# Optimization experiments

Measured on AMD Instinct MI355X. Metric: run time of the kernel, lower is better.

Reference implementation:

```python
import jax, jax.numpy as jnp
import numpy as np

EMBED = 768
HEADS = 12
HEAD_DIM = EMBED // HEADS

def setup_inputs() -> dict:
    key = jax.random.key(0)
    k1, k2, k3, k4 = jax.random.split(key, 4)
    x = jax.random.normal(k1, (8, 1024, EMBED), dtype=jnp.float32)
    # qkv Linear (no bias per qkv_bias=False); proj Linear with bias
    w_qkv = jax.random.normal(k2, (EMBED, 3 * EMBED), dtype=jnp.float32) * 0.02
    w_proj = jax.random.normal(k3, (EMBED, EMBED), dtype=jnp.float32) * 0.02
    b_proj = jax.random.normal(k4, (EMBED,), dtype=jnp.float32) * 0.02
    return {"x": x, "w_qkv": w_qkv, "w_proj": w_proj, "b_proj": b_proj}

def reference(x, w_qkv, w_proj, b_proj):
    b, n, e = x.shape
    h, d = HEADS, HEAD_DIM
    scale = d ** (-0.5)
    qkv = x @ w_qkv                                    # [b, n, 3*e]
    qkv = qkv.reshape(b, n, 3, h, d)                   # (qkv h d) split order
    q, k, v = (jnp.transpose(qkv[:, :, i], (0, 2, 1, 3)) for i in range(3))  # [b,h,n,d]
    dots = jnp.einsum('bhid,bhjd->bhij', q, k) * scale
    attn = jax.nn.softmax(dots, axis=-1)               # dropout p=0 -> identity
    out = jnp.einsum('bhij,bhjd->bhid', attn, v)       # [b,h,n,d]
    out = jnp.transpose(out, (0, 2, 1, 3)).reshape(b, n, e)
    return out @ w_proj + b_proj
```

## Files before the change

kernel.cpp:

```cpp
#include <hip/hip_runtime.h>

typedef _Float16 f16;
typedef _Float16 half8 __attribute__((ext_vector_type(8)));
typedef _Float16 half4v __attribute__((ext_vector_type(4)));
typedef __fp16 fp16x2 __attribute__((ext_vector_type(2)));
typedef float f32x4 __attribute__((ext_vector_type(4)));
typedef float f32x16 __attribute__((ext_vector_type(16)));
typedef unsigned uint4v __attribute__((ext_vector_type(4)));

#define MFMA16(a,b,c) __builtin_amdgcn_mfma_f32_16x16x32_f16((a),(b),(c),0,0,0)
#define MFMA32(a,b,c) __builtin_amdgcn_mfma_f32_32x32x16_f16((a),(b),(c),0,0,0)

__device__ __forceinline__ void gload_lds16(const f16* g, f16* l) {
    __builtin_amdgcn_global_load_lds(
        (const __attribute__((address_space(1))) unsigned int*)g,
        (__attribute__((address_space(3))) unsigned int*)l, 16, 0, 0);
}

__device__ __forceinline__ void plswap(unsigned &a, unsigned &b) {
    asm volatile("v_permlane32_swap_b32 %0, %1" : "+v"(a), "+v"(b));
}

__device__ __forceinline__ unsigned pk2(float a, float b) {
    return __builtin_bit_cast(unsigned, __builtin_amdgcn_cvt_pkrtz(a, b));
}

__device__ __forceinline__ float fexp2(float x) {
#if __has_builtin(__builtin_amdgcn_exp2f)
    return __builtin_amdgcn_exp2f(x);
#else
    return exp2f(x);
#endif
}

__device__ __forceinline__ float xswap32(float x, int hi) {
    unsigned a = __builtin_bit_cast(unsigned, x), b = a;
    asm volatile("v_permlane32_swap_b32 %0, %1" : "+v"(a), "+v"(b));
    return __builtin_bit_cast(float, hi ? a : b);
}

__global__ void cast_f32_to_f16(const float* __restrict__ in, f16* __restrict__ out, int n4) {
    int i = blockIdx.x * blockDim.x + threadIdx.x;
    if (i < n4) {
        float4 v = ((const float4*)in)[i];
        half4v h;
        h.x = (f16)v.x; h.y = (f16)v.y; h.z = (f16)v.z; h.w = (f16)v.w;
        ((half4v*)out)[i] = h;
    }
}

__global__ void transpose_cast(const float* __restrict__ in, f16* __restrict__ out, int K, int N) {
    __shared__ f16 tile[32][33];
    int n0 = blockIdx.x * 32, k0 = blockIdx.y * 32;
    int tx = threadIdx.x & 31, ty = threadIdx.x >> 5;
    for (int r = ty; r < 32; r += 8)
        tile[r][tx] = (f16)in[(size_t)(k0 + r) * N + (n0 + tx)];
    __syncthreads();
    for (int r = ty; r < 32; r += 8)
        out[(size_t)(n0 + r) * K + (k0 + tx)] = tile[tx][r];
}

__global__ __launch_bounds__(256, 3)
void gemm_qkv(const f16* __restrict__ A, const f16* __restrict__ Bt,
              f16* __restrict__ qbuf, f16* __restrict__ kbuf, f16* __restrict__ vtbuf)
{
    constexpr int K = 768;
    constexpr int NX = 18;
    constexpr int NWG = NX * 64;
    __shared__ __align__(16) char smem[49152];
    f16* As = (f16*)smem;
    f16* Bs = (f16*)(smem + 24576);
    const int tid  = threadIdx.x;
    const int lane = tid & 63, wave = tid >> 6;
    const int wm = wave >> 1, wn = wave & 1;
    const int l15 = lane & 15, l4 = lane >> 4;

    const int bid = blockIdx.x;
    const int swz = (bid & 7) * (NWG / 8) + (bid >> 3);
    const int m0 = (swz / NX) * 128, n0 = (swz % NX) * 128;

    const int srow  = lane >> 2;
    const int sslot = lane & 3;

    f32x4 acc[4][4] = {};

    #define GSTAGE(buf, kt) do {                                                     \
        _Pragma("unroll")                                                            \
        for (int i = 0; i < 2; ++i) {                                                \
            int rbase = i * 64 + wave * 16;                                          \
            int row = rbase + srow;                                                  \
            gload_lds16(A  + (size_t)(m0 + row) * K + (kt) + sslot * 8, &As[(buf) * 4096 + rbase * 32]); \
            gload_lds16(Bt + (size_t)(n0 + row) * K + (kt) + sslot * 8, &Bs[(buf) * 4096 + rbase * 32]); \
        }                                                                            \
    } while (0)

    GSTAGE(0, 0);
    GSTAGE(1, 32);

    int cur = 0;
    for (int t = 0; t < 24; ++t) {
        if (t < 23) asm volatile("s_waitcnt vmcnt(4)" ::: "memory");
        else        asm volatile("s_waitcnt vmcnt(0)" ::: "memory");
        __builtin_amdgcn_s_barrier();
        if (t < 22) {
            int nb = cur + 2; if (nb >= 3) nb -= 3;
            GSTAGE(nb, (t + 2) * 32);
        }
        half8 af[4], bf[4];
        #pragma unroll
        for (int mi = 0; mi < 4; mi++) af[mi] = *(const half8*)&As[cur*4096 + (wm*64 + mi*16 + l15) * 32 + l4*8];
        #pragma unroll
        for (int ni = 0; ni < 4; ni++) bf[ni] = *(const half8*)&Bs[cur*4096 + (wn*64 + ni*16 + l15) * 32 + l4*8];
        #pragma unroll
        for (int mi = 0; mi < 4; mi++)
            #pragma unroll
            for (int ni = 0; ni < 4; ni++)
                acc[mi][ni] = MFMA16(af[mi], bf[ni], acc[mi][ni]);
        if (++cur >= 3) cur = 0;
    }
    #undef GSTAGE

    __syncthreads();
    f16* sC = (f16*)smem;
    const int t3 = n0 / 768;
    const int bb = m0 >> 10;
    const int mo = m0 & 1023;
    const int h0 = (n0 - t3 * 768) >> 6;

    if (t3 < 2) {
        #pragma unroll
        for (int mi = 0; mi < 4; mi++)
            #pragma unroll
            for (int ni = 0; ni < 4; ni++)
                #pragma unroll
                for (int r = 0; r < 4; r++) {
                    int row = wm*64 + mi*16 + l4*4 + r;
                    int col = wn*64 + ni*16 + l15;
                    sC[row * 136 + col] = (f16)acc[mi][ni][r];
                }
        __syncthreads();
        f16* outb = (t3 == 0) ? qbuf : kbuf;
        #pragma unroll
        for (int hc = 0; hc < 2; hc++) {
            f16* base = outb + ((size_t)(bb * 12 + h0 + hc) * 1024 + mo) * 64;
            #pragma unroll
            for (int i = 0; i < 4; i++) {
                int row = wave * 32 + i * 8 + (lane >> 3);
                int cc  = (lane & 7) * 8;
                half8 v = *(const half8*)&sC[row * 136 + hc * 64 + cc];
                *(half8*)(base + row * 64 + cc) = v;
            }
        }
    } else {
        #pragma unroll
        for (int mi = 0; mi < 4; mi++)
            #pragma unroll
            for (int ni = 0; ni < 4; ni++) {
                int row0 = wm*64 + mi*16 + l4*4;
                int col  = wn*64 + ni*16 + l15;
                half4v pk;
                #pragma unroll
                for (int r = 0; r < 4; r++) pk[r] = (f16)acc[mi][ni][r];
                *(half4v*)&sC[col * 136 + row0] = pk;
            }
        __syncthreads();
        #pragma unroll
        for (int i = 0; i < 8; i++) {
            int col = wave * 32 + i * 4 + (lane >> 4);
            int rc  = (lane & 15) * 8;
            half8 v = *(const half8*)&sC[col * 136 + rc];
            int head = h0 + (col >> 6), dd = col & 63;
            *(half8*)(vtbuf + ((size_t)(bb * 12 + head) * 64 + dd) * 1024 + mo + rc) = v;
        }
    }
}

__global__ __launch_bounds__(256, 4)
void gemm_proj(const f16* __restrict__ A, const f16* __restrict__ Bt,
               float* __restrict__ out, const float* __restrict__ bias)
{
    constexpr int K = 768;
    constexpr int NX = 12;
    constexpr int NWG = 64 * NX;
    __shared__ __align__(16) char smem[36864];
    f16* As = (f16*)smem;
    f16* Bs = (f16*)(smem + 24576);
    const int tid  = threadIdx.x;
    const int lane = tid & 63, wave = tid >> 6;
    const int wm = wave >> 1, wn = wave & 1;
    const int l15 = lane & 15, l4 = lane >> 4;

    const int bid = blockIdx.x;
    const int swz = (bid & 7) * (NWG / 8) + (bid >> 3);
    const int m0 = (swz / NX) * 128, n0 = (swz % NX) * 64;

    const int srow  = lane >> 2;
    const int sslot = lane & 3;

    f32x4 acc[4][2] = {};

    #define GSTAGE(buf, kt) do {                                                     \
        _Pragma("unroll")                                                            \
        for (int i = 0; i < 2; ++i) {                                                \
            int rbase = i * 64 + wave * 16;                                          \
            gload_lds16(A + (size_t)(m0 + rbase + srow) * K + (kt) + sslot * 8,      \
                        &As[(buf) * 4096 + rbase * 32]);                             \
        }                                                                            \
        gload_lds16(Bt + (size_t)(n0 + wave * 16 + srow) * K + (kt) + sslot * 8,     \
                    &Bs[(buf) * 2048 + wave * 16 * 32]);                             \
    } while (0)

    GSTAGE(0, 0);
    GSTAGE(1, 32);

    int cur = 0;
    for (int t = 0; t < 24; ++t) {
        if (t < 23) asm volatile("s_waitcnt vmcnt(3)" ::: "memory");
        else        asm volatile("s_waitcnt vmcnt(0)" ::: "memory");
        __builtin_amdgcn_s_barrier();
        if (t < 22) {
            int nb = cur + 2; if (nb >= 3) nb -= 3;
            GSTAGE(nb, (t + 2) * 32);
        }
        half8 af[4], bf[2];
        #pragma unroll
        for (int mi = 0; mi < 4; mi++) af[mi] = *(const half8*)&As[cur*4096 + (wm*64 + mi*16 + l15) * 32 + l4*8];
        #pragma unroll
        for (int ni = 0; ni < 2; ni++) bf[ni] = *(const half8*)&Bs[cur*2048 + (wn*32 + ni*16 + l15) * 32 + l4*8];
        #pragma unroll
        for (int mi = 0; mi < 4; mi++)
            #pragma unroll
            for (int ni = 0; ni < 2; ni++)
                acc[mi][ni] = MFMA16(af[mi], bf[ni], acc[mi][ni]);
        if (++cur >= 3) cur = 0;
    }
    #undef GSTAGE

    #pragma unroll
    for (int mi = 0; mi < 4; mi++)
        #pragma unroll
        for (int ni = 0; ni < 2; ni++)
            #pragma unroll
            for (int r = 0; r < 4; r++) {
                int gm = m0 + wm*64 + mi*16 + l4*4 + r;
                int gn = n0 + wn*32 + ni*16 + l15;
                out[(size_t)gm * 768 + gn] = acc[mi][ni][r] + bias[gn];
            }
}

__global__ __launch_bounds__(256, 3)
void attn_kernel(const f16* __restrict__ qbuf, const f16* __restrict__ kbuf,
                 const f16* __restrict__ vtbuf, f16* __restrict__ obuf)
{
    __shared__ __align__(16) f16 Ks[3][4096];
    __shared__ __align__(16) f16 Vs[3][4096];
    const int tid = threadIdx.x;
    const int lane = tid & 63, wave = tid >> 6;
    const int bh = blockIdx.x;
    const int b = bh / 12, h = bh % 12;
    const int q0 = blockIdx.y * 128 + wave * 32;
    const int l31 = lane & 31, hi = lane >> 5;
    const int sw0 = (l31 & 7) << 4;

    const f16* Q  = qbuf  + (size_t)bh * 65536;
    const f16* Kp = kbuf  + (size_t)bh * 65536;
    const f16* Vt = vtbuf + (size_t)bh * 65536;

    const f16 slh = (f16)(0.125f * 1.44269504089f);
    half8 aq[4];
    #pragma unroll
    for (int c = 0; c < 4; c++) {
        aq[c] = *(const half8*)&Q[(size_t)(q0 + l31) * 64 + c * 16 + hi * 8];
        #pragma unroll
        for (int j = 0; j < 8; j++) aq[c][j] *= slh;
    }

    const int srow8 = lane >> 3;
    const int c16   = (lane & 7) ^ srow8;

    f32x16 o0 = {}, o1 = {};
    float lrq = 0.f, mrq = 0.f, stale = 0.f;

    #define STAGE(buf, kv) do {                                                     \
        _Pragma("unroll")                                                           \
        for (int i = 0; i < 2; ++i) {                                               \
            int rbase = wave * 16 + i * 8;                                          \
            int rl = rbase + srow8;                                                 \
            gload_lds16(Kp + (size_t)((kv) + rl) * 64 + c16 * 8, &Ks[buf][rbase * 64]); \
            gload_lds16(Vt + (size_t)rl * 1024 + (kv) + c16 * 8, &Vs[buf][rbase * 64]); \
        }                                                                           \
    } while (0)

    #define QKISSUE(dst0, dst1, kb, minit) do {                                     \
        _Pragma("unroll")                                                           \
        for (int j = 0; j < 16; j++) { dst0[j] = (minit); dst1[j] = (minit); }      \
        __builtin_amdgcn_s_setprio(1);                                              \
        _Pragma("unroll")                                                           \
        for (int c = 0; c < 4; c++) {                                               \
            int koff = (c * 32 + hi * 16) ^ sw0;                                    \
            half8 k0 = *(const half8*)((kb) + l31 * 128 + koff);                    \
            half8 k1 = *(const half8*)((kb) + (32 + l31) * 128 + koff);             \
            dst0 = MFMA32(k0, aq[c], dst0);                                         \
            dst1 = MFMA32(k1, aq[c], dst1);                                         \
        }                                                                           \
        __builtin_amdgcn_s_setprio(0);                                              \
    } while (0)

    STAGE(0, 0);
    STAGE(1, 64);
    __syncthreads();

    f32x16 st0, st1;
    QKISSUE(st0, st1, (const char*)&Ks[0][0], 0.f);

    int bcur = 0;
    for (int t = 0; t < 16; ++t) {
        int bn1 = bcur + 1; if (bn1 >= 3) bn1 -= 3;
        int bn2 = bcur + 2; if (bn2 >= 3) bn2 -= 3;

        if (t < 14) STAGE(bn2, (t + 2) * 64);

        f32x16 sN0, sN1;
        if (t < 15) QKISSUE(sN0, sN1, (const char*)&Ks[bn1][0], -mrq);

        if (__any(stale != 0.f)) {
            #pragma unroll
            for (int j = 0; j < 16; j++) { st0[j] -= stale; st1[j] -= stale; }
        }
        stale = 0.f;

        float m16;
        {
            float p0 = fmaxf(fmaxf(st0[0],  st0[1]),  fmaxf(st0[2],  st0[3]));
            float p1 = fmaxf(fmaxf(st0[4],  st0[5]),  fmaxf(st0[6],  st0[7]));
            float p2 = fmaxf(fmaxf(st0[8],  st0[9]),  fmaxf(st0[10], st0[11]));
            float p3 = fmaxf(fmaxf(st0[12], st0[13]), fmaxf(st0[14], st0[15]));
            float r0 = fmaxf(fmaxf(st1[0],  st1[1]),  fmaxf(st1[2],  st1[3]));
            float r1 = fmaxf(fmaxf(st1[4],  st1[5]),  fmaxf(st1[6],  st1[7]));
            float r2 = fmaxf(fmaxf(st1[8],  st1[9]),  fmaxf(st1[10], st1[11]));
            float r3 = fmaxf(fmaxf(st1[12], st1[13]), fmaxf(st1[14], st1[15]));
            m16 = fmaxf(fmaxf(fmaxf(p0, p1), fmaxf(p2, p3)),
                        fmaxf(fmaxf(r0, r1), fmaxf(r2, r3)));
        }
        m16 = fmaxf(m16, xswap32(m16, hi));

        if (!__all(m16 <= 11.0f)) {
            float d = fmaxf(m16, 0.f);
            float alpha = fexp2(-d);
            mrq += d;
            stale = d;
            #pragma unroll
            for (int j = 0; j < 16; j++) { st0[j] -= d; st1[j] -= d; }
            lrq *= alpha;
            #pragma unroll
            for (int reg = 0; reg < 16; reg++) {
                float a = __shfl(alpha, (reg & 3) + 8 * (reg >> 2) + 4 * hi);
                o0[reg] *= a; o1[reg] *= a;
            }
        }

        float rs = 0.f;
        half8 pa[4];
        #pragma unroll
        for (int tile = 0; tile < 2; tile++) {
            const f32x16& sv = tile ? st1 : st0;
            #pragma unroll
            for (int half16 = 0; half16 < 2; half16++) {
                int rb = half16 * 8;
                unsigned A1, B1, A2, B2;
                {
                    float e0 = fexp2(sv[rb+0]), e1 = fexp2(sv[rb+1]);
                    float e4 = fexp2(sv[rb+4]), e5 = fexp2(sv[rb+5]);
                    rs += (e0 + e1) + (e4 + e5);
                    A1 = pk2(e0, e1); B1 = pk2(e4, e5);
                    plswap(A1, B1);
                }
                {
                    float e2 = fexp2(sv[rb+2]), e3 = fexp2(sv[rb+3]);
                    float e6 = fexp2(sv[rb+6]), e7 = fexp2(sv[rb+7]);
                    rs += (e2 + e3) + (e6 + e7);
                    A2 = pk2(e2, e3); B2 = pk2(e6, e7);
                    plswap(A2, B2);
                }
                uint4v w = {A1, A2, B1, B2};
                pa[tile * 2 + half16] = __builtin_bit_cast(half8, w);
            }
        }
        rs += xswap32(rs, hi);
        lrq += rs;

        {
            const char* Vb = (const char*)&Vs[bcur][0];
            __builtin_amdgcn_s_setprio(1);
            #pragma unroll
            for (int kc = 0; kc < 4; kc++) {
                int koff = (kc * 32 + hi * 16) ^ sw0;
                half8 v0 = *(const half8*)(Vb + l31 * 128 + koff);
                half8 v1 = *(const half8*)(Vb + (32 + l31) * 128 + koff);
                o0 = MFMA32(pa[kc], v0, o0);
                o1 = MFMA32(pa[kc], v1, o1);
            }
            __builtin_amdgcn_s_setprio(0);
        }

        if (t < 15) {
            asm volatile("s_waitcnt vmcnt(0)" ::: "memory");
            __builtin_amdgcn_s_barrier();
            st0 = sN0; st1 = sN1;
        }
        bcur = bn1;
    }
    #undef QKISSUE
    #undef STAGE

    float rq = 1.0f / lrq;
    f16* Op = obuf + (size_t)b * 1024 * 768 + h * 64;
    #pragma unroll
    for (int reg = 0; reg < 16; reg++) {
        int qrow = (reg & 3) + 8 * (reg >> 2) + 4 * hi;
        float inv = __shfl(rq, qrow);
        size_t base = (size_t)(q0 + qrow) * 768;
        Op[base + l31]      = (f16)(o0[reg] * inv);
        Op[base + 32 + l31] = (f16)(o1[reg] * inv);
    }
}

extern "C" void kernel_launch(void* const* d_in, const int* in_sizes, int n_in,
                              void* d_out, int out_size, void* d_ws, size_t ws_size,
                              hipStream_t stream) {
    const float* x      = (const float*)d_in[0];
    const float* w_qkv  = (const float*)d_in[1];
    const float* w_proj = (const float*)d_in[2];
    const float* b_proj = (const float*)d_in[3];
    float* out = (float*)d_out;
    char* ws = (char*)d_ws;

    f16* x_h      = (f16*)(ws + 0);
    f16* w_qkv_t  = (f16*)(ws + 12582912);
    f16* w_proj_t = (f16*)(ws + 16121856);
    f16* qb       = (f16*)(ws + 17301504);
    f16* kb       = (f16*)(ws + 29884416);
    f16* vtb      = (f16*)(ws + 42467328);
    f16* ob       = (f16*)(ws + 55050240);

    cast_f32_to_f16<<<dim3(6144), dim3(256), 0, stream>>>(x, x_h, 6291456 / 4);
    transpose_cast<<<dim3(2304 / 32, 768 / 32), dim3(256), 0, stream>>>(w_qkv, w_qkv_t, 768, 2304);
    transpose_cast<<<dim3(768 / 32, 768 / 32), dim3(256), 0, stream>>>(w_proj, w_proj_t, 768, 768);
    gemm_qkv<<<dim3(18 * 64), dim3(256), 0, stream>>>(x_h, w_qkv_t, qb, kb, vtb);
    attn_kernel<<<dim3(96, 8), dim3(256), 0, stream>>>(qb, kb, vtb, ob);
    gemm_proj<<<dim3(12 * 64), dim3(256), 0, stream>>>(ob, w_proj_t, out, b_proj);
}
```

Measured before the change: 123.5 us.

## Merge prep kernels, double-buffer qkv GEMM for occupancy, widen proj tiles

Three preprocessing launches (x cast plus two weight transpose-casts) become one prep kernel that picks its task from the block index, removing launch overhead. The QKV GEMM drops from a three-stage to a two-stage LDS buffer with plain __syncthreads and a half-tile epilogue, so shared memory falls from 48KB to 32KB and launch bounds rise to 5 blocks per CU. The proj GEMM switches from 128x64 to 128x128 tiles with three-stage buffering, halving its grid to 384 blocks. Tradeoffs: less latency hiding in the QKV loop, extra barriers in its epilogue, and fewer proj blocks to fill the GPU.

```diff
diff --git a/kernel.cpp b/kernel.cpp
--- a/kernel.cpp
+++ b/kernel.cpp
@@ -39,19 +39,25 @@
     return __builtin_bit_cast(float, hi ? a : b);
 }
 
-__global__ void cast_f32_to_f16(const float* __restrict__ in, f16* __restrict__ out, int n4) {
-    int i = blockIdx.x * blockDim.x + threadIdx.x;
-    if (i < n4) {
-        float4 v = ((const float4*)in)[i];
+__global__ void prep_kernel(const float* __restrict__ x, f16* __restrict__ x_h,
+                            const float* __restrict__ w_qkv, f16* __restrict__ w_qkv_t,
+                            const float* __restrict__ w_proj, f16* __restrict__ w_proj_t)
+{
+    __shared__ f16 tile[32][33];
+    const int bidx = blockIdx.x;
+    if (bidx < 6144) {
+        int i = bidx * 256 + threadIdx.x;
+        float4 v = ((const float4*)x)[i];
         half4v h;
         h.x = (f16)v.x; h.y = (f16)v.y; h.z = (f16)v.z; h.w = (f16)v.w;
-        ((half4v*)out)[i] = h;
-    }
-}
-
-__global__ void transpose_cast(const float* __restrict__ in, f16* __restrict__ out, int K, int N) {
-    __shared__ f16 tile[32][33];
-    int n0 = blockIdx.x * 32, k0 = blockIdx.y * 32;
+        ((half4v*)x_h)[i] = h;
+        return;
+    }
+    const float* in;  f16* out;  int N, idx;
+    if (bidx < 6144 + 1728) { idx = bidx - 6144; in = w_qkv;  out = w_qkv_t;  N = 2304; }
+    else                    { idx = bidx - 7872; in = w_proj; out = w_proj_t; N = 768;  }
+    const int K = 768;
+    int n0 = (idx % (N / 32)) * 32, k0 = (idx / (N / 32)) * 32;
     int tx = threadIdx.x & 31, ty = threadIdx.x >> 5;
     for (int r = ty; r < 32; r += 8)
         tile[r][tx] = (f16)in[(size_t)(k0 + r) * N + (n0 + tx)];
@@ -60,16 +66,16 @@
         out[(size_t)(n0 + r) * K + (k0 + tx)] = tile[tx][r];
 }
 
-__global__ __launch_bounds__(256, 3)
+__global__ __launch_bounds__(256, 5)
 void gemm_qkv(const f16* __restrict__ A, const f16* __restrict__ Bt,
               f16* __restrict__ qbuf, f16* __restrict__ kbuf, f16* __restrict__ vtbuf)
 {
     constexpr int K = 768;
     constexpr int NX = 18;
     constexpr int NWG = NX * 64;
-    __shared__ __align__(16) char smem[49152];
+    __shared__ __align__(16) char smem[32768];
     f16* As = (f16*)smem;
-    f16* Bs = (f16*)(smem + 24576);
+    f16* Bs = (f16*)(smem + 16384);
     const int tid  = threadIdx.x;
     const int lane = tid & 63, wave = tid >> 6;
     const int wm = wave >> 1, wn = wave & 1;
@@ -95,6 +101,128 @@
     } while (0)
 
     GSTAGE(0, 0);
+    __syncthreads();
+
+    for (int t = 0; t < 24; ++t) {
+        const int cur = t & 1;
+        if (t < 23) GSTAGE(cur ^ 1, (t + 1) * 32);
+        half8 af[4], bf[4];
+        #pragma unroll
+        for (int mi = 0; mi < 4; mi++) af[mi] = *(const half8*)&As[cur*4096 + (wm*64 + mi*16 + l15) * 32 + l4*8];
+        #pragma unroll
+        for (int ni = 0; ni < 4; ni++) bf[ni] = *(const half8*)&Bs[cur*4096 + (wn*64 + ni*16 + l15) * 32 + l4*8];
+        #pragma unroll
+        for (int mi = 0; mi < 4; mi++)
+            #pragma unroll
+            for (int ni = 0; ni < 4; ni++)
+                acc[mi][ni] = MFMA16(af[mi], bf[ni], acc[mi][ni]);
+        __syncthreads();
+    }
+    #undef GSTAGE
+
+    const int t3 = n0 / 768;
+    const int bb = m0 >> 10;
+    const int mo = m0 & 1023;
+    const int h0 = (n0 - t3 * 768) >> 6;
+
+    if (t3 < 2) {
+        f16* sC = (f16*)smem;
+        f16* outb = (t3 == 0) ? qbuf : kbuf;
+        #pragma unroll
+        for (int hh = 0; hh < 2; hh++) {
+            if (wm == hh) {
+                #pragma unroll
+                for (int mi = 0; mi < 4; mi++)
+                    #pragma unroll
+                    for (int ni = 0; ni < 4; ni++)
+                        #pragma unroll
+                        for (int r = 0; r < 4; r++) {
+                            int row = mi*16 + l4*4 + r;
+                            int col = wn*64 + ni*16 + l15;
+                            sC[row * 136 + col] = (f16)acc[mi][ni][r];
+                        }
+            }
+            __syncthreads();
+            #pragma unroll
+            for (int hc = 0; hc < 2; hc++) {
+                f16* base = outb + ((size_t)(bb * 12 + h0 + hc) * 1024 + mo + hh * 64) * 64;
+                #pragma unroll
+                for (int i = 0; i < 2; i++) {
+                    int row = i * 32 + (tid >> 3);
+                    int cc  = (tid & 7) * 8;
+                    half8 v = *(const half8*)&sC[row * 136 + hc * 64 + cc];
+                    *(half8*)(base + row * 64 + cc) = v;
+                }
+            }
+            __syncthreads();
+        }
+    } else {
+        f16* sC = (f16*)smem;
+        #pragma unroll
+        for (int hh = 0; hh < 2; hh++) {
+            if (wn == hh) {
+                #pragma unroll
+                for (int mi = 0; mi < 4; mi++)
+                    #pragma unroll
+                    for (int ni = 0; ni < 4; ni++) {
+                        int row0 = wm*64 + mi*16 + l4*4;
+                        int col  = ni*16 + l15;
+                        half4v pk;
+                        #pragma unroll
+                        for (int r = 0; r < 4; r++) pk[r] = (f16)acc[mi][ni][r];
+                        *(half4v*)&sC[col * 136 + row0] = pk;
+                    }
+            }
+            __syncthreads();
+            #pragma unroll
+            for (int i = 0; i < 4; i++) {
+                int col = i * 16 + (tid >> 4);
+                int rc  = (tid & 15) * 8;
+                half8 v = *(const half8*)&sC[col * 136 + rc];
+                int colg = hh * 64 + col;
+                int head = h0 + (colg >> 6), dd = colg & 63;
+                *(half8*)(vtbuf + ((size_t)(bb * 12 + head) * 64 + dd) * 1024 + mo + rc) = v;
+            }
+            __syncthreads();
+        }
+    }
+}
+
+__global__ __launch_bounds__(256, 3)
+void gemm_proj(const f16* __restrict__ A, const f16* __restrict__ Bt,
+               float* __restrict__ out, const float* __restrict__ bias)
+{
+    constexpr int K = 768;
+    constexpr int NX = 6;
+    constexpr int NWG = NX * 64;
+    __shared__ __align__(16) char smem[49152];
+    f16* As = (f16*)smem;
+    f16* Bs = (f16*)(smem + 24576);
+    const int tid  = threadIdx.x;
+    const int lane = tid & 63, wave = tid >> 6;
+    const int wm = wave >> 1, wn = wave & 1;
+    const int l15 = lane & 15, l4 = lane >> 4;
+
+    const int bid = blockIdx.x;
+    const int swz = (bid & 7) * (NWG / 8) + (bid >> 3);
+    const int m0 = (swz / NX) * 128, n0 = (swz % NX) * 128;
+
+    const int srow  = lane >> 2;
+    const int sslot = lane & 3;
+
+    f32x4 acc[4][4] = {};
+
+    #define GSTAGE(buf, kt) do {                                                     \
+        _Pragma("unroll")                                                            \
+        for (int i = 0; i < 2; ++i) {                                                \
+            int rbase = i * 64 + wave * 16;                                          \
+            int row = rbase + srow;                                                  \
+            gload_lds16(A  + (size_t)(m0 + row) * K + (kt) + sslot * 8, &As[(buf) * 4096 + rbase * 32]); \
+            gload_lds16(Bt + (size_t)(n0 + row) * K + (kt) + sslot * 8, &Bs[(buf) * 4096 + rbase * 32]); \
+        }                                                                            \
+    } while (0)
+
+    GSTAGE(0, 0);
     GSTAGE(1, 32);
 
     int cur = 0;
@@ -120,130 +248,14 @@
     }
     #undef GSTAGE
 
-    __syncthreads();
-    f16* sC = (f16*)smem;
-    const int t3 = n0 / 768;
-    const int bb = m0 >> 10;
-    const int mo = m0 & 1023;
-    const int h0 = (n0 - t3 * 768) >> 6;
-
-    if (t3 < 2) {
-        #pragma unroll
-        for (int mi = 0; mi < 4; mi++)
-            #pragma unroll
-            for (int ni = 0; ni < 4; ni++)
-                #pragma unroll
-                for (int r = 0; r < 4; r++) {
-                    int row = wm*64 + mi*16 + l4*4 + r;
-                    int col = wn*64 + ni*16 + l15;
-                    sC[row * 136 + col] = (f16)acc[mi][ni][r];
-                }
-        __syncthreads();
-        f16* outb = (t3 == 0) ? qbuf : kbuf;
-        #pragma unroll
-        for (int hc = 0; hc < 2; hc++) {
-            f16* base = outb + ((size_t)(bb * 12 + h0 + hc) * 1024 + mo) * 64;
-            #pragma unroll
-            for (int i = 0; i < 4; i++) {
-                int row = wave * 32 + i * 8 + (lane >> 3);
-                int cc  = (lane & 7) * 8;
-                half8 v = *(const half8*)&sC[row * 136 + hc * 64 + cc];
-                *(half8*)(base + row * 64 + cc) = v;
-            }
-        }
-    } else {
-        #pragma unroll
-        for (int mi = 0; mi < 4; mi++)
-            #pragma unroll
-            for (int ni = 0; ni < 4; ni++) {
-                int row0 = wm*64 + mi*16 + l4*4;
-                int col  = wn*64 + ni*16 + l15;
-                half4v pk;
-                #pragma unroll
-                for (int r = 0; r < 4; r++) pk[r] = (f16)acc[mi][ni][r];
-                *(half4v*)&sC[col * 136 + row0] = pk;
-            }
-        __syncthreads();
-        #pragma unroll
-        for (int i = 0; i < 8; i++) {
-            int col = wave * 32 + i * 4 + (lane >> 4);
-            int rc  = (lane & 15) * 8;
-            half8 v = *(const half8*)&sC[col * 136 + rc];
-            int head = h0 + (col >> 6), dd = col & 63;
-            *(half8*)(vtbuf + ((size_t)(bb * 12 + head) * 64 + dd) * 1024 + mo + rc) = v;
-        }
-    }
-}
-
-__global__ __launch_bounds__(256, 4)
-void gemm_proj(const f16* __restrict__ A, const f16* __restrict__ Bt,
-               float* __restrict__ out, const float* __restrict__ bias)
-{
-    constexpr int K = 768;
-    constexpr int NX = 12;
-    constexpr int NWG = 64 * NX;
-    __shared__ __align__(16) char smem[36864];
-    f16* As = (f16*)smem;
-    f16* Bs = (f16*)(smem + 24576);
-    const int tid  = threadIdx.x;
-    const int lane = tid & 63, wave = tid >> 6;
-    const int wm = wave >> 1, wn = wave & 1;
-    const int l15 = lane & 15, l4 = lane >> 4;
-
-    const int bid = blockIdx.x;
-    const int swz = (bid & 7) * (NWG / 8) + (bid >> 3);
-    const int m0 = (swz / NX) * 128, n0 = (swz % NX) * 64;
-
-    const int srow  = lane >> 2;
-    const int sslot = lane & 3;
-
-    f32x4 acc[4][2] = {};
-
-    #define GSTAGE(buf, kt) do {                                                     \
-        _Pragma("unroll")                                                            \
-        for (int i = 0; i < 2; ++i) {                                                \
-            int rbase = i * 64 + wave * 16;                                          \
-            gload_lds16(A + (size_t)(m0 + rbase + srow) * K + (kt) + sslot * 8,      \
-                        &As[(buf) * 4096 + rbase * 32]);                             \
-        }                                                                            \
-        gload_lds16(Bt + (size_t)(n0 + wave * 16 + srow) * K + (kt) + sslot * 8,     \
-                    &Bs[(buf) * 2048 + wave * 16 * 32]);                             \
-    } while (0)
-
-    GSTAGE(0, 0);
-    GSTAGE(1, 32);
-
-    int cur = 0;
-    for (int t = 0; t < 24; ++t) {
-        if (t < 23) asm volatile("s_waitcnt vmcnt(3)" ::: "memory");
-        else        asm volatile("s_waitcnt vmcnt(0)" ::: "memory");
-        __builtin_amdgcn_s_barrier();
-        if (t < 22) {
-            int nb = cur + 2; if (nb >= 3) nb -= 3;
-            GSTAGE(nb, (t + 2) * 32);
-        }
-        half8 af[4], bf[2];
-        #pragma unroll
-        for (int mi = 0; mi < 4; mi++) af[mi] = *(const half8*)&As[cur*4096 + (wm*64 + mi*16 + l15) * 32 + l4*8];
-        #pragma unroll
-        for (int ni = 0; ni < 2; ni++) bf[ni] = *(const half8*)&Bs[cur*2048 + (wn*32 + ni*16 + l15) * 32 + l4*8];
-        #pragma unroll
-        for (int mi = 0; mi < 4; mi++)
-            #pragma unroll
-            for (int ni = 0; ni < 2; ni++)
-                acc[mi][ni] = MFMA16(af[mi], bf[ni], acc[mi][ni]);
-        if (++cur >= 3) cur = 0;
-    }
-    #undef GSTAGE
-
     #pragma unroll
     for (int mi = 0; mi < 4; mi++)
         #pragma unroll
-        for (int ni = 0; ni < 2; ni++)
+        for (int ni = 0; ni < 4; ni++)
             #pragma unroll
             for (int r = 0; r < 4; r++) {
                 int gm = m0 + wm*64 + mi*16 + l4*4 + r;
-                int gn = n0 + wn*32 + ni*16 + l15;
+                int gn = n0 + wn*64 + ni*16 + l15;
                 out[(size_t)gm * 768 + gn] = acc[mi][ni][r] + bias[gn];
             }
 }
@@ -443,10 +455,9 @@
     f16* vtb      = (f16*)(ws + 42467328);
     f16* ob       = (f16*)(ws + 55050240);
 
-    cast_f32_to_f16<<<dim3(6144), dim3(256), 0, stream>>>(x, x_h, 6291456 / 4);
-    transpose_cast<<<dim3(2304 / 32, 768 / 32), dim3(256), 0, stream>>>(w_qkv, w_qkv_t, 768, 2304);
-    transpose_cast<<<dim3(768 / 32, 768 / 32), dim3(256), 0, stream>>>(w_proj, w_proj_t, 768, 768);
+    prep_kernel<<<dim3(6144 + 1728 + 576), dim3(256), 0, stream>>>(
+        x, x_h, w_qkv, w_qkv_t, w_proj, w_proj_t);
     gemm_qkv<<<dim3(18 * 64), dim3(256), 0, stream>>>(x_h, w_qkv_t, qb, kb, vtb);
     attn_kernel<<<dim3(96, 8), dim3(256), 0, stream>>>(qb, kb, vtb, ob);
-    gemm_proj<<<dim3(12 * 64), dim3(256), 0, stream>>>(ob, w_proj_t, out, b_proj);
-}
+    gemm_proj<<<dim3(6 * 64), dim3(256), 0, stream>>>(ob, w_proj_t, out, b_proj);
+}
```

After: 142.1 us. 1.15x slower.
